# Kernel optimization log

Hardware: AMD Instinct MI355X
Metric: run time of the kernel (lower is better)

Reference implementation:

```python
import jax, jax.numpy as jnp
import numpy as np

B, S, D = 2, 1024, 1024   # batch, seq, hidden_dim
E, K, I = 16, 4, 512      # num_experts, top-k, expert intermediate_dim


def setup_inputs() -> dict:
    key = jax.random.key(0)
    kx, kr, kg, ku, kd = jax.random.split(key, 5)
    x = jax.random.normal(kx, (B, S, D), dtype=jnp.float32)
    # _init_weight: std = 1/sqrt(fan_in), truncated normal in [-3, 3]
    router = (1.0 / np.sqrt(D)) * jax.random.truncated_normal(kr, -3, 3, (D, E), dtype=jnp.float32)
    router_bias = jnp.zeros((E,), dtype=jnp.float32)
    w_gate = (1.0 / np.sqrt(D)) * jax.random.truncated_normal(kg, -3, 3, (E, D, I), dtype=jnp.float32)
    w_up = (1.0 / np.sqrt(D)) * jax.random.truncated_normal(ku, -3, 3, (E, D, I), dtype=jnp.float32)
    w_gate_up = jnp.concatenate([w_gate, w_up], axis=-1)  # (E, D, 2I)
    # _init_down_proj: std = 1/(alpha_ffn * sqrt(hidden_dim)), alpha_ffn = I/D
    std_down = 1.0 / ((I / D) * np.sqrt(D))
    w_down = std_down * jax.random.truncated_normal(kd, -3, 3, (E, I, D), dtype=jnp.float32)
    return {"x": x, "router": router, "router_bias": router_bias,
            "w_gate_up": w_gate_up, "w_down": w_down}


def reference(x, router, router_bias, w_gate_up, w_down):
    b, s, d = x.shape
    T = b * s
    x_flat = x.reshape(T, d)                                   # (T, D)

    # Router: biased logits for selection, unbiased for combine weights.
    router_logits = jnp.einsum('td,de->te', x_flat, router)     # (T, E)
    biased = router_logits + jax.lax.stop_gradient(router_bias)
    _, selected = jax.lax.top_k(biased, K)                      # (T, K) int32
    unbiased_topk = jnp.take_along_axis(router_logits, selected, axis=-1)
    topk_w = jax.nn.sigmoid(unbiased_topk)
    combine_w = (topk_w / jnp.sum(topk_w, axis=-1, keepdims=True)).astype(x.dtype)

    # Routing stats.
    counts = jnp.sum(jax.nn.one_hot(selected, E, dtype=jnp.float32), axis=(0, 1))
    total = jnp.maximum(jnp.sum(counts), 1.0)
    frac = counts / total
    entropy = -jnp.sum(frac * jnp.log(frac + 1e-06))

    # Dense dispatch: scatter top-k weights into a (T, E) combine matrix
    # (zeros for unselected experts => identical math, dropless).
    combine = jnp.zeros((T, E), x.dtype).at[jnp.arange(T)[:, None], selected].add(combine_w)

    # Expert MLPs: SiGLU with fused gate/up projection.
    gu = jnp.einsum('td,edh->teh', x_flat, w_gate_up)           # (T, E, 2I)
    g, u = jnp.split(gu, 2, axis=-1)
    h = (jax.nn.silu(g) * u) * combine[:, :, None]              # (T, E, I), weighted
    y = jnp.einsum('tei,eid->td', h, w_down)                    # (T, D)

    routed = y.reshape(b, s, d)
    return (routed, counts, entropy)
```

## Files before the change

### kernel.cpp

```cpp
#include <hip/hip_runtime.h>
#include <hip/hip_bf16.h>
#include <cstdint>

#define T_TOK 2048
#define D_DIM 1024
#define E_NUM 16
#define K_TOP 4
#define I_DIM 512
#define TWOI  1024
#define RTPB  8

typedef __bf16 bf16x8 __attribute__((ext_vector_type(8)));
typedef __bf16 bf16x4 __attribute__((ext_vector_type(4)));
typedef float  f32x4  __attribute__((ext_vector_type(4)));

__device__ __forceinline__ void gload_lds16(const void* g, void* l) {
    __builtin_amdgcn_global_load_lds(
        (const __attribute__((address_space(1))) void*)(uintptr_t)(g),
        (__attribute__((address_space(3))) void*)(uintptr_t)(l),
        16, 0, 0);
}

__global__ __launch_bounds__(256) void transpose_router_kernel(
    const float* __restrict__ router, float* __restrict__ routerT)
{
    const int i = blockIdx.x * 256 + threadIdx.x;
    const int e = i & 15, d = i >> 4;
    routerT[(size_t)e * D_DIM + d] = router[i];
}

__global__ __launch_bounds__(256) void router_fast_kernel(
    const float* __restrict__ x, const float* __restrict__ routerT,
    const float* __restrict__ rbias,
    int* __restrict__ sel_idx, float* __restrict__ sel_w, int* __restrict__ counts)
{
    __shared__ float4 xs[RTPB * 256];
    __shared__ float lgs[RTPB][E_NUM];
    const int tid = threadIdx.x;
    const int t0 = blockIdx.x * RTPB;

    const float4* xg = reinterpret_cast<const float4*>(x + (size_t)t0 * D_DIM);
#pragma unroll
    for (int j = 0; j < RTPB; ++j) xs[tid + j * 256] = xg[tid + j * 256];
    __syncthreads();

    const int tok = tid >> 5, sub = tid & 31, half = sub >> 4, e = sub & 15;
    const float4* xr = xs + tok * 256 + half * 128;
    const float4* rr = reinterpret_cast<const float4*>(routerT + (size_t)e * D_DIM) + half * 128;
    float4 a = make_float4(0.f, 0.f, 0.f, 0.f);
#pragma unroll 8
    for (int i = 0; i < 128; ++i) {
        const float4 xv = xr[i], rv = rr[i];
        a.x += xv.x * rv.x; a.y += xv.y * rv.y;
        a.z += xv.z * rv.z; a.w += xv.w * rv.w;
    }
    float acc = (a.x + a.y) + (a.z + a.w);
    acc += __shfl_xor(acc, 16);
    if (half == 0) lgs[tok][e] = acc;
    __syncthreads();

    if (tid < RTPB) {
        const int t = t0 + tid;
        float lg[E_NUM], bi[E_NUM];
#pragma unroll
        for (int j = 0; j < E_NUM; ++j) { lg[j] = lgs[tid][j]; bi[j] = lg[j] + rbias[j]; }
        bool used[E_NUM];
#pragma unroll
        for (int j = 0; j < E_NUM; ++j) used[j] = false;
        int selv[K_TOP]; float wvv[K_TOP]; float wsum = 0.f;
#pragma unroll
        for (int k = 0; k < K_TOP; ++k) {
            float best = -1e30f; int bidx = 0;
#pragma unroll
            for (int j = 0; j < E_NUM; ++j)
                if (!used[j] && bi[j] > best) { best = bi[j]; bidx = j; }
            used[bidx] = true; selv[k] = bidx;
            const float s = 1.f / (1.f + expf(-lg[bidx]));
            wvv[k] = s; wsum += s;
        }
#pragma unroll
        for (int k = 0; k < K_TOP; ++k) {
            sel_idx[t * K_TOP + k] = selv[k];
            sel_w[t * K_TOP + k] = wvv[k] / wsum;
            atomicAdd(&counts[selv[k]], 1);
        }
    }
}

__global__ __launch_bounds__(256) void router_wave_kernel(
    const float* __restrict__ x, const float* __restrict__ router,
    const float* __restrict__ rbias,
    int* __restrict__ sel_idx, float* __restrict__ sel_w, int* __restrict__ counts)
{
    const int wv = threadIdx.x >> 6;
    const int lane = threadIdx.x & 63;
    const int t = blockIdx.x * 4 + wv;
    if (t >= T_TOK) return;
    const int e = lane & 15, dg = lane >> 4;

    const float* xp = x + (size_t)t * D_DIM + dg * 256;
    const float* rp = router + (size_t)(dg * 256) * E_NUM + e;
    float acc = 0.f;
#pragma unroll 4
    for (int i = 0; i < 256; ++i) acc += xp[i] * rp[i * E_NUM];
    acc += __shfl_xor(acc, 16);
    acc += __shfl_xor(acc, 32);

    float lg[E_NUM], bi[E_NUM];
#pragma unroll
    for (int j = 0; j < E_NUM; ++j) {
        lg[j] = __shfl(acc, j);
        bi[j] = lg[j] + rbias[j];
    }
    bool used[E_NUM];
#pragma unroll
    for (int j = 0; j < E_NUM; ++j) used[j] = false;
    int selv[K_TOP]; float wvv[K_TOP]; float wsum = 0.f;
#pragma unroll
    for (int k = 0; k < K_TOP; ++k) {
        float best = -1e30f; int bidx = 0;
#pragma unroll
        for (int j = 0; j < E_NUM; ++j)
            if (!used[j] && bi[j] > best) { best = bi[j]; bidx = j; }
#pragma unroll
        for (int j = 0; j < E_NUM; ++j) if (j == bidx) used[j] = true;
        selv[k] = bidx;
        float lgv = 0.f;
#pragma unroll
        for (int j = 0; j < E_NUM; ++j) if (j == bidx) lgv = lg[j];
        const float s = 1.f / (1.f + expf(-lgv));
        wvv[k] = s; wsum += s;
    }
    if (lane == 0) {
#pragma unroll
        for (int k = 0; k < K_TOP; ++k) {
            sel_idx[t * K_TOP + k] = selv[k];
            sel_w[t * K_TOP + k] = wvv[k] / wsum;
            atomicAdd(&counts[selv[k]], 1);
        }
    }
}

__global__ void scan_stats_kernel(const int* __restrict__ counts,
                                  int* __restrict__ offsets, int* __restrict__ cursor,
                                  float* __restrict__ out_tail)
{
    if (threadIdx.x == 0 && blockIdx.x == 0) {
        int off = 0; float tot = 0.f;
        for (int e = 0; e < E_NUM; ++e) {
            offsets[e] = off; cursor[e] = off; off += counts[e];
            tot += (float)counts[e];
        }
        offsets[E_NUM] = off;
        const float total = fmaxf(tot, 1.f);
        float ent = 0.f;
        for (int e = 0; e < E_NUM; ++e) {
            const float c = (float)counts[e];
            const float frac = c / total;
            ent -= frac * logf(frac + 1e-6f);
            out_tail[e] = c;
        }
        out_tail[E_NUM] = ent;
    }
}

__global__ void scatter_kernel(const int* __restrict__ sel_idx,
                               int* __restrict__ cursor, int* __restrict__ perm)
{
    const int i = blockIdx.x * 256 + threadIdx.x;
    if (i >= T_TOK * K_TOP) return;
    const int e = sel_idx[i];
    const int pos = atomicAdd(&cursor[e], 1);
    perm[pos] = i;
}

__global__ __launch_bounds__(256) void convert_x_kernel(
    const float* __restrict__ x, __bf16* __restrict__ xb)
{
    const int i = blockIdx.x * 256 + threadIdx.x;
    const float4 a = reinterpret_cast<const float4*>(x)[i * 2];
    const float4 b = reinterpret_cast<const float4*>(x)[i * 2 + 1];
    bf16x8 o;
    o[0] = (__bf16)a.x; o[1] = (__bf16)a.y; o[2] = (__bf16)a.z; o[3] = (__bf16)a.w;
    o[4] = (__bf16)b.x; o[5] = (__bf16)b.y; o[6] = (__bf16)b.z; o[7] = (__bf16)b.w;
    reinterpret_cast<bf16x8*>(xb)[i] = o;
}

__global__ __launch_bounds__(256) void transpose_w_kernel(
    const float* __restrict__ in, __bf16* __restrict__ out, int R, int C)
{
    const int e = blockIdx.z;
    const int r0 = blockIdx.y * 32, c0 = blockIdx.x * 32;
    const int tid = threadIdx.x;
    const int r = tid >> 3, c4 = (tid & 7) * 4;
    __shared__ float lds[32][33];
    const float4 v = *reinterpret_cast<const float4*>(
        in + (size_t)e * R * C + (size_t)(r0 + r) * C + c0 + c4);
    lds[c4 + 0][r] = v.x; lds[c4 + 1][r] = v.y;
    lds[c4 + 2][r] = v.z; lds[c4 + 3][r] = v.w;
    __syncthreads();
    bf16x4 o;
    o[0] = (__bf16)lds[r][c4 + 0]; o[1] = (__bf16)lds[r][c4 + 1];
    o[2] = (__bf16)lds[r][c4 + 2]; o[3] = (__bf16)lds[r][c4 + 3];
    *reinterpret_cast<bf16x4*>(out + (size_t)e * R * C + (size_t)(c0 + r) * R + r0 + c4) = o;
}

__global__ __launch_bounds__(256) void gate_mfma_kernel(
    const __bf16* __restrict__ xb, const __bf16* __restrict__ wguT,
    const int* __restrict__ offsets, const int* __restrict__ perm,
    const float* __restrict__ sel_w, __bf16* __restrict__ h)
{
    const int e = blockIdx.z;
    const int base = offsets[e];
    const int nrows = offsets[e + 1] - base;
    const int m0 = blockIdx.y * 128;
    if (m0 >= nrows) return;
    const int c0 = blockIdx.x * 64;

    __shared__ __align__(16) __bf16 As[128 * 32];
    __shared__ __align__(16) __bf16 Bg[64 * 32];
    __shared__ __align__(16) __bf16 Bu[64 * 32];
    __shared__ int   tokrow[128];
    __shared__ float wrow[128];

    const int tid = threadIdx.x;
    const int wv = tid >> 6, lane = tid & 63;

    if (tid < 128) {
        const int gr = m0 + tid;
        const int grc = min(gr, nrows - 1);
        const int pv = perm[base + grc];
        tokrow[tid] = pv >> 2;
        wrow[tid] = (gr < nrows) ? sel_w[pv] : 0.f;
    }
    __syncthreads();

    const int ca0 = wv * 64 + lane, ca1 = 256 + wv * 64 + lane;
    const int ra0 = ca0 >> 2, ka0 = (ca0 & 3) ^ (ra0 & 3);
    const int ra1 = ca1 >> 2, ka1 = (ca1 & 3) ^ (ra1 & 3);
    const __bf16* a_src0 = xb + (size_t)tokrow[ra0] * D_DIM + ka0 * 8;
    const __bf16* a_src1 = xb + (size_t)tokrow[ra1] * D_DIM + ka1 * 8;
    const int cb = wv * 64 + lane;
    const int rb = cb >> 2, kb = (cb & 3) ^ (rb & 3);
    const size_t wbase = (size_t)e * D_DIM * TWOI;
    const __bf16* bg_src = wguT + wbase + (size_t)(c0 + rb) * D_DIM + kb * 8;
    const __bf16* bu_src = wguT + wbase + (size_t)(c0 + 512 + rb) * D_DIM + kb * 8;
    __bf16* a_dst0 = As + wv * 512;
    __bf16* a_dst1 = As + 2048 + wv * 512;
    __bf16* bg_dst = Bg + wv * 512;
    __bf16* bu_dst = Bu + wv * 512;

    const int wr = wv >> 1, wc = wv & 1;
    int a_off[4], b_off[2];
#pragma unroll
    for (int m = 0; m < 4; ++m) {
        const int row = wr * 64 + m * 16 + (lane & 15);
        a_off[m] = row * 32 + (((lane >> 4) ^ (row & 3)) << 3);
    }
#pragma unroll
    for (int n = 0; n < 2; ++n) {
        const int col = wc * 32 + n * 16 + (lane & 15);
        b_off[n] = col * 32 + (((lane >> 4) ^ (col & 3)) << 3);
    }

    f32x4 accg[4][2] = {}; f32x4 accu[4][2] = {};
    for (int d0 = 0; d0 < D_DIM; d0 += 32) {
        gload_lds16(a_src0 + d0, a_dst0);
        gload_lds16(a_src1 + d0, a_dst1);
        gload_lds16(bg_src + d0, bg_dst);
        gload_lds16(bu_src + d0, bu_dst);
        __syncthreads();
        bf16x8 af[4], bgf[2], buf[2];
#pragma unroll
        for (int m = 0; m < 4; ++m) af[m] = *reinterpret_cast<const bf16x8*>(&As[a_off[m]]);
#pragma unroll
        for (int n = 0; n < 2; ++n) {
            bgf[n] = *reinterpret_cast<const bf16x8*>(&Bg[b_off[n]]);
            buf[n] = *reinterpret_cast<const bf16x8*>(&Bu[b_off[n]]);
        }
#pragma unroll
        for (int m = 0; m < 4; ++m)
#pragma unroll
            for (int n = 0; n < 2; ++n) {
                accg[m][n] = __builtin_amdgcn_mfma_f32_16x16x32_bf16(af[m], bgf[n], accg[m][n], 0, 0, 0);
                accu[m][n] = __builtin_amdgcn_mfma_f32_16x16x32_bf16(af[m], buf[n], accu[m][n], 0, 0, 0);
            }
        __syncthreads();
    }

#pragma unroll
    for (int m = 0; m < 4; ++m)
#pragma unroll
        for (int n = 0; n < 2; ++n)
#pragma unroll
            for (int j = 0; j < 4; ++j) {
                const int lr = wr * 64 + m * 16 + (lane >> 4) * 4 + j;
                const int gr = m0 + lr;
                if (gr < nrows) {
                    const int col = c0 + wc * 32 + n * 16 + (lane & 15);
                    const float g = accg[m][n][j];
                    const float u = accu[m][n][j];
                    const float s = g / (1.f + expf(-g));
                    h[(size_t)(base + gr) * I_DIM + col] = (__bf16)(s * u * wrow[lr]);
                }
            }
}

__global__ __launch_bounds__(256) void down_mfma_kernel(
    const __bf16* __restrict__ h, const __bf16* __restrict__ wdnT,
    const int* __restrict__ offsets, const int* __restrict__ perm,
    float* __restrict__ y)
{
    const int e = blockIdx.z;
    const int base = offsets[e];
    const int nrows = offsets[e + 1] - base;
    const int m0 = blockIdx.y * 128;
    if (m0 >= nrows) return;
    const int c0 = blockIdx.x * 128;

    __shared__ __align__(16) __bf16 As[128 * 32];
    __shared__ __align__(16) __bf16 Bs[128 * 32];
    __shared__ int tokrow[128];

    const int tid = threadIdx.x;
    const int wv = tid >> 6, lane = tid & 63;

    if (tid < 128) {
        const int gr = m0 + tid;
        const int grc = min(gr, nrows - 1);
        tokrow[tid] = perm[base + grc] >> 2;
    }
    __syncthreads();

    const int ca0 = wv * 64 + lane, ca1 = 256 + wv * 64 + lane;
    const int ra0 = ca0 >> 2, ka0 = (ca0 & 3) ^ (ra0 & 3);
    const int ra1 = ca1 >> 2, ka1 = (ca1 & 3) ^ (ra1 & 3);
    const __bf16* a_src0 = h + (size_t)(base + min(m0 + ra0, nrows - 1)) * I_DIM + ka0 * 8;
    const __bf16* a_src1 = h + (size_t)(base + min(m0 + ra1, nrows - 1)) * I_DIM + ka1 * 8;
    const size_t wbase = (size_t)e * I_DIM * D_DIM;
    const __bf16* b_src0 = wdnT + wbase + (size_t)(c0 + ra0) * I_DIM + ka0 * 8;
    const __bf16* b_src1 = wdnT + wbase + (size_t)(c0 + ra1) * I_DIM + ka1 * 8;
    __bf16* a_dst0 = As + wv * 512;
    __bf16* a_dst1 = As + 2048 + wv * 512;
    __bf16* b_dst0 = Bs + wv * 512;
    __bf16* b_dst1 = Bs + 2048 + wv * 512;

    const int wr = wv >> 1, wc = wv & 1;
    int a_off[4], b_off[4];
#pragma unroll
    for (int m = 0; m < 4; ++m) {
        const int row = wr * 64 + m * 16 + (lane & 15);
        a_off[m] = row * 32 + (((lane >> 4) ^ (row & 3)) << 3);
        const int col = wc * 64 + m * 16 + (lane & 15);
        b_off[m] = col * 32 + (((lane >> 4) ^ (col & 3)) << 3);
    }

    f32x4 acc[4][4] = {};
    for (int d0 = 0; d0 < I_DIM; d0 += 32) {
        gload_lds16(a_src0 + d0, a_dst0);
        gload_lds16(a_src1 + d0, a_dst1);
        gload_lds16(b_src0 + d0, b_dst0);
        gload_lds16(b_src1 + d0, b_dst1);
        __syncthreads();
        bf16x8 af[4], bf[4];
#pragma unroll
        for (int m = 0; m < 4; ++m) {
            af[m] = *reinterpret_cast<const bf16x8*>(&As[a_off[m]]);
            bf[m] = *reinterpret_cast<const bf16x8*>(&Bs[b_off[m]]);
        }
#pragma unroll
        for (int m = 0; m < 4; ++m)
#pragma unroll
            for (int n = 0; n < 4; ++n)
                acc[m][n] = __builtin_amdgcn_mfma_f32_16x16x32_bf16(af[m], bf[n], acc[m][n], 0, 0, 0);
        __syncthreads();
    }

#pragma unroll
    for (int m = 0; m < 4; ++m)
#pragma unroll
        for (int j = 0; j < 4; ++j) {
            const int lr = wr * 64 + m * 16 + (lane >> 4) * 4 + j;
            const int gr = m0 + lr;
            if (gr < nrows) {
                const int tok = tokrow[lr];
#pragma unroll
                for (int n = 0; n < 4; ++n) {
                    const int col = c0 + wc * 64 + n * 16 + (lane & 15);
                    atomicAdd(&y[(size_t)tok * D_DIM + col], acc[m][n][j]);
                }
            }
        }
}

__global__ __launch_bounds__(256) void gate_gemm_kernel(
    const float* __restrict__ x, const float* __restrict__ wgu,
    const int* __restrict__ offsets, const int* __restrict__ perm,
    const float* __restrict__ sel_w, float* __restrict__ h)
{
    const int e = blockIdx.z;
    const int base = offsets[e];
    const int nrows = offsets[e + 1] - base;
    const int m0 = blockIdx.y * 64;
    if (m0 >= nrows) return;
    const int c0 = blockIdx.x * 64;
    const int tid = threadIdx.x;
    __shared__ float As[16][64];
    __shared__ float Bg[16][64];
    __shared__ float Bu[16][64];
    const int lrow = tid >> 2;
    const int c4 = (tid & 3) * 4;
    const int grow = m0 + lrow;
    const bool arow_ok = (grow < nrows);
    const float* xrow = nullptr;
    if (arow_ok) {
        const int pv = perm[base + grow];
        xrow = x + (size_t)(pv >> 2) * D_DIM;
    }
    const int bcol = tid & 63;
    const int brow0 = tid >> 6;
    const float* wbase = wgu + (size_t)e * D_DIM * TWOI;
    const int tx = tid & 15, ty = tid >> 4;
    float accg[4][4] = {}, accu[4][4] = {};
    for (int d0 = 0; d0 < D_DIM; d0 += 16) {
        float4 av = make_float4(0.f, 0.f, 0.f, 0.f);
        if (arow_ok) av = *reinterpret_cast<const float4*>(xrow + d0 + c4);
        As[c4 + 0][lrow] = av.x; As[c4 + 1][lrow] = av.y;
        As[c4 + 2][lrow] = av.z; As[c4 + 3][lrow] = av.w;
#pragma unroll
        for (int r = 0; r < 4; ++r) {
            const int dd = d0 + brow0 + r * 4;
            const float* wr = wbase + (size_t)dd * TWOI;
            Bg[brow0 + r * 4][bcol] = wr[c0 + bcol];
            Bu[brow0 + r * 4][bcol] = wr[c0 + 512 + bcol];
        }
        __syncthreads();
#pragma unroll
        for (int kk = 0; kk < 16; ++kk) {
            const float4 a  = *reinterpret_cast<const float4*>(&As[kk][ty * 4]);
            const float4 bg = *reinterpret_cast<const float4*>(&Bg[kk][tx * 4]);
            const float4 bu = *reinterpret_cast<const float4*>(&Bu[kk][tx * 4]);
            const float aa[4] = { a.x, a.y, a.z, a.w };
            const float gg[4] = { bg.x, bg.y, bg.z, bg.w };
            const float uu[4] = { bu.x, bu.y, bu.z, bu.w };
#pragma unroll
            for (int i2 = 0; i2 < 4; ++i2)
#pragma unroll
                for (int j = 0; j < 4; ++j) {
                    accg[i2][j] += aa[i2] * gg[j];
                    accu[i2][j] += aa[i2] * uu[j];
                }
        }
        __syncthreads();
    }
#pragma unroll
    for (int i2 = 0; i2 < 4; ++i2) {
        const int r = ty * 4 + i2;
        const int gr = m0 + r;
        if (gr < nrows) {
            const int pv = perm[base + gr];
            const float wgt = sel_w[pv];
            float* hrow = h + (size_t)(base + gr) * I_DIM + c0;
#pragma unroll
            for (int j = 0; j < 4; ++j) {
                const float g = accg[i2][j];
                const float u = accu[i2][j];
                const float s = g / (1.f + expf(-g));
                hrow[tx * 4 + j] = s * u * wgt;
            }
        }
    }
}

__global__ __launch_bounds__(256) void down_gemm_kernel(
    const float* __restrict__ h, const float* __restrict__ wdn,
    const int* __restrict__ offsets, const int* __restrict__ perm,
    float* __restrict__ y)
{
    const int e = blockIdx.z;
    const int base = offsets[e];
    const int nrows = offsets[e + 1] - base;
    const int m0 = blockIdx.y * 64;
    if (m0 >= nrows) return;
    const int c0 = blockIdx.x * 64;
    const int tid = threadIdx.x;
    __shared__ float As[16][64];
    __shared__ float Bs[16][64];
    const int lrow = tid >> 2;
    const int c4 = (tid & 3) * 4;
    const int grow = m0 + lrow;
    const bool arow_ok = (grow < nrows);
    const float* hrow = arow_ok ? (h + (size_t)(base + grow) * I_DIM) : nullptr;
    const int bcol = tid & 63;
    const int brow0 = tid >> 6;
    const float* wbase = wdn + (size_t)e * I_DIM * D_DIM;
    const int tx = tid & 15, ty = tid >> 4;
    float acc[4][4] = {};
    for (int d0 = 0; d0 < I_DIM; d0 += 16) {
        float4 av = make_float4(0.f, 0.f, 0.f, 0.f);
        if (arow_ok) av = *reinterpret_cast<const float4*>(hrow + d0 + c4);
        As[c4 + 0][lrow] = av.x; As[c4 + 1][lrow] = av.y;
        As[c4 + 2][lrow] = av.z; As[c4 + 3][lrow] = av.w;
#pragma unroll
        for (int r = 0; r < 4; ++r) {
            const int dd = d0 + brow0 + r * 4;
            Bs[brow0 + r * 4][bcol] = wbase[(size_t)dd * D_DIM + c0 + bcol];
        }
        __syncthreads();
#pragma unroll
        for (int kk = 0; kk < 16; ++kk) {
            const float4 a = *reinterpret_cast<const float4*>(&As[kk][ty * 4]);
            const float4 b = *reinterpret_cast<const float4*>(&Bs[kk][tx * 4]);
            const float aa[4] = { a.x, a.y, a.z, a.w };
            const float bb[4] = { b.x, b.y, b.z, b.w };
#pragma unroll
            for (int i2 = 0; i2 < 4; ++i2)
#pragma unroll
                for (int j = 0; j < 4; ++j)
                    acc[i2][j] += aa[i2] * bb[j];
        }
        __syncthreads();
    }
#pragma unroll
    for (int i2 = 0; i2 < 4; ++i2) {
        const int r = ty * 4 + i2;
        const int gr = m0 + r;
        if (gr < nrows) {
            const int pv = perm[base + gr];
            const int t = pv >> 2;
            float* yrow = y + (size_t)t * D_DIM + c0;
#pragma unroll
            for (int j = 0; j < 4; ++j)
                atomicAdd(&yrow[tx * 4 + j], acc[i2][j]);
        }
    }
}

extern "C" void kernel_launch(void* const* d_in, const int* in_sizes, int n_in,
                              void* d_out, int out_size, void* d_ws, size_t ws_size,
                              hipStream_t stream)
{
    const float* x      = (const float*)d_in[0];
    const float* router = (const float*)d_in[1];
    const float* rbias  = (const float*)d_in[2];
    const float* wgu    = (const float*)d_in[3];
    const float* wdn    = (const float*)d_in[4];
    float* out = (float*)d_out;

    char* ws = (char*)d_ws;
    int*   sel_idx = (int*)(ws);
    float* sel_w   = (float*)(ws + 32768);
    int*   perm    = (int*)(ws + 65536);
    int*   counts  = (int*)(ws + 98304);
    int*   offsets = (int*)(ws + 98560);
    int*   cursor  = (int*)(ws + 98816);
    __bf16* xb   = (__bf16*)(ws + 131072);
    __bf16* hb   = (__bf16*)(ws + 4325376);
    __bf16* wguT = (__bf16*)(ws + 12713984);
    __bf16* wdnT = (__bf16*)(ws + 46268416);
    float* routerT = (float*)(ws + 63045632);
    float* hf    = (float*)(ws + 131072);

    const bool fast = (ws_size >= 63111168ULL);

    hipMemsetAsync(counts, 0, 64, stream);
    hipMemsetAsync(out, 0, (size_t)T_TOK * D_DIM * sizeof(float), stream);

    if (fast) {
        transpose_router_kernel<<<64, 256, 0, stream>>>(router, routerT);
        router_fast_kernel<<<T_TOK / RTPB, 256, 0, stream>>>(x, routerT, rbias, sel_idx, sel_w, counts);
    } else {
        router_wave_kernel<<<T_TOK / 4, 256, 0, stream>>>(x, router, rbias, sel_idx, sel_w, counts);
    }
    scan_stats_kernel<<<1, 64, 0, stream>>>(counts, offsets, cursor,
                                            out + (size_t)T_TOK * D_DIM);
    scatter_kernel<<<(T_TOK * K_TOP + 255) / 256, 256, 0, stream>>>(sel_idx, cursor, perm);

    if (fast) {
        convert_x_kernel<<<T_TOK * D_DIM / 8 / 256, 256, 0, stream>>>(x, xb);
        transpose_w_kernel<<<dim3(TWOI / 32, D_DIM / 32, E_NUM), 256, 0, stream>>>(wgu, wguT, D_DIM, TWOI);
        transpose_w_kernel<<<dim3(D_DIM / 32, I_DIM / 32, E_NUM), 256, 0, stream>>>(wdn, wdnT, I_DIM, D_DIM);
        gate_mfma_kernel<<<dim3(8, 16, E_NUM), 256, 0, stream>>>(xb, wguT, offsets, perm, sel_w, hb);
        down_mfma_kernel<<<dim3(8, 16, E_NUM), 256, 0, stream>>>(hb, wdnT, offsets, perm, out);
    } else {
        gate_gemm_kernel<<<dim3(8, 32, E_NUM), 256, 0, stream>>>(x, wgu, offsets, perm, sel_w, hf);
        down_gemm_kernel<<<dim3(16, 32, E_NUM), 256, 0, stream>>>(hf, wdn, offsets, perm, out);
    }
}
```

Baseline: 297.5 us.

## Replace atomic down-projection scatter with per-slot partials plus gather-combine kernel

The down projection now writes each routed row's partial output to a per-slot buffer, and a new combine kernel sums the four partials per token through an inverse permutation recorded in the scatter kernel. This removes the atomic accumulation into the output and the full output memset. The gate kernel and the new down kernel use narrower column tiles, doubling the grid to raise occupancy. In exchange it needs a larger workspace (about 32 MB more) and an extra kernel launch that reads the partials back. It falls back to the old path when the workspace is too small.

```diff
diff --git a/kernel.cpp b/kernel.cpp
--- a/kernel.cpp
+++ b/kernel.cpp
@@ -165,13 +165,15 @@
 }
 
 __global__ void scatter_kernel(const int* __restrict__ sel_idx,
-                               int* __restrict__ cursor, int* __restrict__ perm)
+                               int* __restrict__ cursor, int* __restrict__ perm,
+                               int* __restrict__ inv)
 {
     const int i = blockIdx.x * 256 + threadIdx.x;
     if (i >= T_TOK * K_TOP) return;
     const int e = sel_idx[i];
     const int pos = atomicAdd(&cursor[e], 1);
     perm[pos] = i;
+    inv[i] = pos;
 }
 
 __global__ __launch_bounds__(256) void convert_x_kernel(
@@ -215,11 +217,11 @@
     const int nrows = offsets[e + 1] - base;
     const int m0 = blockIdx.y * 128;
     if (m0 >= nrows) return;
-    const int c0 = blockIdx.x * 64;
+    const int c0 = blockIdx.x * 32;
 
     __shared__ __align__(16) __bf16 As[128 * 32];
-    __shared__ __align__(16) __bf16 Bg[64 * 32];
-    __shared__ __align__(16) __bf16 Bu[64 * 32];
+    __shared__ __align__(16) __bf16 Bg[32 * 32];
+    __shared__ __align__(16) __bf16 Bu[32 * 32];
     __shared__ int   tokrow[128];
     __shared__ float wrow[128];
 
@@ -235,75 +237,158 @@
     }
     __syncthreads();
 
-    const int ca0 = wv * 64 + lane, ca1 = 256 + wv * 64 + lane;
+    const int ca0 = tid, ca1 = 256 + tid;
     const int ra0 = ca0 >> 2, ka0 = (ca0 & 3) ^ (ra0 & 3);
     const int ra1 = ca1 >> 2, ka1 = (ca1 & 3) ^ (ra1 & 3);
     const __bf16* a_src0 = xb + (size_t)tokrow[ra0] * D_DIM + ka0 * 8;
     const __bf16* a_src1 = xb + (size_t)tokrow[ra1] * D_DIM + ka1 * 8;
-    const int cb = wv * 64 + lane;
-    const int rb = cb >> 2, kb = (cb & 3) ^ (rb & 3);
+    const int cbl = tid & 127;
+    const int rb = cbl >> 2, kb = (cbl & 3) ^ (rb & 3);
     const size_t wbase = (size_t)e * D_DIM * TWOI;
-    const __bf16* bg_src = wguT + wbase + (size_t)(c0 + rb) * D_DIM + kb * 8;
-    const __bf16* bu_src = wguT + wbase + (size_t)(c0 + 512 + rb) * D_DIM + kb * 8;
+    const __bf16* b_src = wguT + wbase +
+        (size_t)(c0 + (tid < 128 ? 0 : 512) + rb) * D_DIM + kb * 8;
     __bf16* a_dst0 = As + wv * 512;
     __bf16* a_dst1 = As + 2048 + wv * 512;
-    __bf16* bg_dst = Bg + wv * 512;
-    __bf16* bu_dst = Bu + wv * 512;
+    __bf16* b_dst = (wv < 2 ? Bg + wv * 512 : Bu + (wv - 2) * 512);
 
     const int wr = wv >> 1, wc = wv & 1;
-    int a_off[4], b_off[2];
+    int a_off[4];
 #pragma unroll
     for (int m = 0; m < 4; ++m) {
         const int row = wr * 64 + m * 16 + (lane & 15);
         a_off[m] = row * 32 + (((lane >> 4) ^ (row & 3)) << 3);
     }
+    const int col = wc * 16 + (lane & 15);
+    const int b_off = col * 32 + (((lane >> 4) ^ (col & 3)) << 3);
+
+    f32x4 accg[4] = {}; f32x4 accu[4] = {};
+    for (int d0 = 0; d0 < D_DIM; d0 += 32) {
+        gload_lds16(a_src0 + d0, a_dst0);
+        gload_lds16(a_src1 + d0, a_dst1);
+        gload_lds16(b_src + d0, b_dst);
+        __syncthreads();
+        bf16x8 af[4];
+#pragma unroll
+        for (int m = 0; m < 4; ++m) af[m] = *reinterpret_cast<const bf16x8*>(&As[a_off[m]]);
+        const bf16x8 bgf = *reinterpret_cast<const bf16x8*>(&Bg[b_off]);
+        const bf16x8 buf = *reinterpret_cast<const bf16x8*>(&Bu[b_off]);
+#pragma unroll
+        for (int m = 0; m < 4; ++m) {
+            accg[m] = __builtin_amdgcn_mfma_f32_16x16x32_bf16(af[m], bgf, accg[m], 0, 0, 0);
+            accu[m] = __builtin_amdgcn_mfma_f32_16x16x32_bf16(af[m], buf, accu[m], 0, 0, 0);
+        }
+        __syncthreads();
+    }
+
+    const int ocol = c0 + wc * 16 + (lane & 15);
+#pragma unroll
+    for (int m = 0; m < 4; ++m)
+#pragma unroll
+        for (int j = 0; j < 4; ++j) {
+            const int lr = wr * 64 + m * 16 + (lane >> 4) * 4 + j;
+            const int gr = m0 + lr;
+            if (gr < nrows) {
+                const float g = accg[m][j];
+                const float u = accu[m][j];
+                const float s = g / (1.f + expf(-g));
+                h[(size_t)(base + gr) * I_DIM + ocol] = (__bf16)(s * u * wrow[lr]);
+            }
+        }
+}
+
+__global__ __launch_bounds__(256) void down_mfma_p_kernel(
+    const __bf16* __restrict__ h, const __bf16* __restrict__ wdnT,
+    const int* __restrict__ offsets, float* __restrict__ yp)
+{
+    const int e = blockIdx.z;
+    const int base = offsets[e];
+    const int nrows = offsets[e + 1] - base;
+    const int m0 = blockIdx.y * 128;
+    if (m0 >= nrows) return;
+    const int c0 = blockIdx.x * 64;
+
+    __shared__ __align__(16) __bf16 As[128 * 32];
+    __shared__ __align__(16) __bf16 Bs[64 * 32];
+
+    const int tid = threadIdx.x;
+    const int wv = tid >> 6, lane = tid & 63;
+
+    const int ca0 = tid, ca1 = 256 + tid;
+    const int ra0 = ca0 >> 2, ka0 = (ca0 & 3) ^ (ra0 & 3);
+    const int ra1 = ca1 >> 2, ka1 = (ca1 & 3) ^ (ra1 & 3);
+    const __bf16* a_src0 = h + (size_t)(base + min(m0 + ra0, nrows - 1)) * I_DIM + ka0 * 8;
+    const __bf16* a_src1 = h + (size_t)(base + min(m0 + ra1, nrows - 1)) * I_DIM + ka1 * 8;
+    const int rb = tid >> 2, kb = (tid & 3) ^ (rb & 3);
+    const size_t wbase = (size_t)e * I_DIM * D_DIM;
+    const __bf16* b_src = wdnT + wbase + (size_t)(c0 + rb) * I_DIM + kb * 8;
+    __bf16* a_dst0 = As + wv * 512;
+    __bf16* a_dst1 = As + 2048 + wv * 512;
+    __bf16* b_dst = Bs + wv * 512;
+
+    const int wr = wv >> 1, wc = wv & 1;
+    int a_off[4], b_off[2];
+#pragma unroll
+    for (int m = 0; m < 4; ++m) {
+        const int row = wr * 64 + m * 16 + (lane & 15);
+        a_off[m] = row * 32 + (((lane >> 4) ^ (row & 3)) << 3);
+    }
 #pragma unroll
     for (int n = 0; n < 2; ++n) {
         const int col = wc * 32 + n * 16 + (lane & 15);
         b_off[n] = col * 32 + (((lane >> 4) ^ (col & 3)) << 3);
     }
 
-    f32x4 accg[4][2] = {}; f32x4 accu[4][2] = {};
-    for (int d0 = 0; d0 < D_DIM; d0 += 32) {
+    f32x4 acc[4][2] = {};
+    for (int d0 = 0; d0 < I_DIM; d0 += 32) {
         gload_lds16(a_src0 + d0, a_dst0);
         gload_lds16(a_src1 + d0, a_dst1);
-        gload_lds16(bg_src + d0, bg_dst);
-        gload_lds16(bu_src + d0, bu_dst);
-        __syncthreads();
-        bf16x8 af[4], bgf[2], buf[2];
+        gload_lds16(b_src + d0, b_dst);
+        __syncthreads();
+        bf16x8 af[4], bf[2];
 #pragma unroll
         for (int m = 0; m < 4; ++m) af[m] = *reinterpret_cast<const bf16x8*>(&As[a_off[m]]);
 #pragma unroll
-        for (int n = 0; n < 2; ++n) {
-            bgf[n] = *reinterpret_cast<const bf16x8*>(&Bg[b_off[n]]);
-            buf[n] = *reinterpret_cast<const bf16x8*>(&Bu[b_off[n]]);
-        }
+        for (int n = 0; n < 2; ++n) bf[n] = *reinterpret_cast<const bf16x8*>(&Bs[b_off[n]]);
 #pragma unroll
         for (int m = 0; m < 4; ++m)
 #pragma unroll
-            for (int n = 0; n < 2; ++n) {
-                accg[m][n] = __builtin_amdgcn_mfma_f32_16x16x32_bf16(af[m], bgf[n], accg[m][n], 0, 0, 0);
-                accu[m][n] = __builtin_amdgcn_mfma_f32_16x16x32_bf16(af[m], buf[n], accu[m][n], 0, 0, 0);
-            }
+            for (int n = 0; n < 2; ++n)
+                acc[m][n] = __builtin_amdgcn_mfma_f32_16x16x32_bf16(af[m], bf[n], acc[m][n], 0, 0, 0);
         __syncthreads();
     }
 
 #pragma unroll
     for (int m = 0; m < 4; ++m)
 #pragma unroll
-        for (int n = 0; n < 2; ++n)
-#pragma unroll
-            for (int j = 0; j < 4; ++j) {
-                const int lr = wr * 64 + m * 16 + (lane >> 4) * 4 + j;
-                const int gr = m0 + lr;
-                if (gr < nrows) {
+        for (int j = 0; j < 4; ++j) {
+            const int lr = wr * 64 + m * 16 + (lane >> 4) * 4 + j;
+            const int gr = m0 + lr;
+            if (gr < nrows) {
+#pragma unroll
+                for (int n = 0; n < 2; ++n) {
                     const int col = c0 + wc * 32 + n * 16 + (lane & 15);
-                    const float g = accg[m][n][j];
-                    const float u = accu[m][n][j];
-                    const float s = g / (1.f + expf(-g));
-                    h[(size_t)(base + gr) * I_DIM + col] = (__bf16)(s * u * wrow[lr]);
+                    yp[(size_t)(base + gr) * D_DIM + col] = acc[m][n][j];
                 }
             }
+        }
+}
+
+__global__ __launch_bounds__(256) void combine_kernel(
+    const float* __restrict__ yp, const int* __restrict__ inv, float* __restrict__ y)
+{
+    const int t = blockIdx.x, tid = threadIdx.x;
+    const int r0 = inv[t * 4 + 0], r1 = inv[t * 4 + 1];
+    const int r2 = inv[t * 4 + 2], r3 = inv[t * 4 + 3];
+    const float4 a = reinterpret_cast<const float4*>(yp + (size_t)r0 * D_DIM)[tid];
+    const float4 b = reinterpret_cast<const float4*>(yp + (size_t)r1 * D_DIM)[tid];
+    const float4 c = reinterpret_cast<const float4*>(yp + (size_t)r2 * D_DIM)[tid];
+    const float4 d = reinterpret_cast<const float4*>(yp + (size_t)r3 * D_DIM)[tid];
+    float4 s;
+    s.x = (a.x + b.x) + (c.x + d.x);
+    s.y = (a.y + b.y) + (c.y + d.y);
+    s.z = (a.z + b.z) + (c.z + d.z);
+    s.w = (a.w + b.w) + (c.w + d.w);
+    reinterpret_cast<float4*>(y + (size_t)t * D_DIM)[tid] = s;
 }
 
 __global__ __launch_bounds__(256) void down_mfma_kernel(
@@ -551,22 +636,26 @@
     int*   sel_idx = (int*)(ws);
     float* sel_w   = (float*)(ws + 32768);
     int*   perm    = (int*)(ws + 65536);
-    int*   counts  = (int*)(ws + 98304);
-    int*   offsets = (int*)(ws + 98560);
-    int*   cursor  = (int*)(ws + 98816);
-    __bf16* xb   = (__bf16*)(ws + 131072);
-    __bf16* hb   = (__bf16*)(ws + 4325376);
-    __bf16* wguT = (__bf16*)(ws + 12713984);
-    __bf16* wdnT = (__bf16*)(ws + 46268416);
-    float* routerT = (float*)(ws + 63045632);
-    float* hf    = (float*)(ws + 131072);
-
-    const bool fast = (ws_size >= 63111168ULL);
+    int*   inv     = (int*)(ws + 98304);
+    int*   counts  = (int*)(ws + 131072);
+    int*   offsets = (int*)(ws + 131328);
+    int*   cursor  = (int*)(ws + 131584);
+    __bf16* xb     = (__bf16*)(ws + 262144);
+    __bf16* hb     = (__bf16*)(ws + 4456448);
+    __bf16* wguT   = (__bf16*)(ws + 12845056);
+    __bf16* wdnT   = (__bf16*)(ws + 46399488);
+    float* routerT = (float*)(ws + 63176704);
+    float* yp      = (float*)(ws + 63242240);
+    float* hf      = (float*)(ws + 262144);
+
+    const bool fast = (ws_size >= 96796672ULL);
+    const bool mid  = (ws_size >= 63242240ULL);
 
     hipMemsetAsync(counts, 0, 64, stream);
-    hipMemsetAsync(out, 0, (size_t)T_TOK * D_DIM * sizeof(float), stream);
-
-    if (fast) {
+    if (!fast)
+        hipMemsetAsync(out, 0, (size_t)T_TOK * D_DIM * sizeof(float), stream);
+
+    if (mid) {
         transpose_router_kernel<<<64, 256, 0, stream>>>(router, routerT);
         router_fast_kernel<<<T_TOK / RTPB, 256, 0, stream>>>(x, routerT, rbias, sel_idx, sel_w, counts);
     } else {
@@ -574,14 +663,19 @@
     }
     scan_stats_kernel<<<1, 64, 0, stream>>>(counts, offsets, cursor,
                                             out + (size_t)T_TOK * D_DIM);
-    scatter_kernel<<<(T_TOK * K_TOP + 255) / 256, 256, 0, stream>>>(sel_idx, cursor, perm);
-
-    if (fast) {
+    scatter_kernel<<<(T_TOK * K_TOP + 255) / 256, 256, 0, stream>>>(sel_idx, cursor, perm, inv);
+
+    if (mid) {
         convert_x_kernel<<<T_TOK * D_DIM / 8 / 256, 256, 0, stream>>>(x, xb);
         transpose_w_kernel<<<dim3(TWOI / 32, D_DIM / 32, E_NUM), 256, 0, stream>>>(wgu, wguT, D_DIM, TWOI);
         transpose_w_kernel<<<dim3(D_DIM / 32, I_DIM / 32, E_NUM), 256, 0, stream>>>(wdn, wdnT, I_DIM, D_DIM);
-        gate_mfma_kernel<<<dim3(8, 16, E_NUM), 256, 0, stream>>>(xb, wguT, offsets, perm, sel_w, hb);
-        down_mfma_kernel<<<dim3(8, 16, E_NUM), 256, 0, stream>>>(hb, wdnT, offsets, perm, out);
+        gate_mfma_kernel<<<dim3(16, 16, E_NUM), 256, 0, stream>>>(xb, wguT, offsets, perm, sel_w, hb);
+        if (fast) {
+            down_mfma_p_kernel<<<dim3(16, 16, E_NUM), 256, 0, stream>>>(hb, wdnT, offsets, yp);
+            combine_kernel<<<T_TOK, 256, 0, stream>>>(yp, inv, out);
+        } else {
+            down_mfma_kernel<<<dim3(8, 16, E_NUM), 256, 0, stream>>>(hb, wdnT, offsets, perm, out);
+        }
     } else {
         gate_gemm_kernel<<<dim3(8, 32, E_NUM), 256, 0, stream>>>(x, wgu, offsets, perm, sel_w, hf);
         down_gemm_kernel<<<dim3(16, 32, E_NUM), 256, 0, stream>>>(hf, wdn, offsets, perm, out);
```

Result: no change. 294.6 us (-1.0%).
